# Performance work log

Hardware: AMD Instinct MI355X
Metric: run time of the kernel (lower is better)

Reference implementation:

```python
import jax, jax.numpy as jnp
import numpy as np

N, E, S, G = 524288, 2097152, 8192, 64
F_IN, HID = 64, 128


def setup_inputs() -> dict:
    key = jax.random.key(0)
    ks = jax.random.split(key, 12)
    x = jax.random.normal(ks[0], (N, F_IN), dtype=jnp.float32)
    edge_index = jax.random.randint(ks[1], (2, E), 0, N, dtype=jnp.int64)
    node_batch = jnp.sort(jax.random.randint(ks[2], (N,), 0, S, dtype=jnp.int64))
    weights = jax.random.uniform(ks[3], (S, 1), dtype=jnp.float32)
    subgraph_batch = jnp.sort(jax.random.randint(ks[4], (S,), 0, G, dtype=jnp.int64))
    s = 1.0 / np.sqrt(F_IN)
    h = 1.0 / np.sqrt(HID)
    W_l = jax.random.uniform(ks[5], (F_IN, HID), jnp.float32, -s, s)
    W_r = jax.random.uniform(ks[6], (F_IN, HID), jnp.float32, -s, s)
    b_conv = jax.random.uniform(ks[7], (HID,), jnp.float32, -s, s)
    W1 = jax.random.uniform(ks[8], (HID, HID), jnp.float32, -h, h)
    b1 = jax.random.uniform(ks[9], (HID,), jnp.float32, -h, h)
    W2 = jax.random.uniform(ks[10], (HID, 1), jnp.float32, -h, h)
    b2 = jax.random.uniform(ks[11], (1,), jnp.float32, -h, h)
    return {"x": x, "edge_index": edge_index, "node_batch": node_batch,
            "weights": weights, "subgraph_batch": subgraph_batch,
            "W_l": W_l, "W_r": W_r, "b_conv": b_conv,
            "W1": W1, "b1": b1, "W2": W2, "b2": b2}


def reference(x, edge_index, node_batch, weights, subgraph_batch,
              W_l, W_r, b_conv, W1, b1, W2, b2):
    src, dst = edge_index[0], edge_index[1]
    # GraphSAGE mean aggregation: gather neighbor feats, scatter-mean to dst
    msg_sum = jax.ops.segment_sum(x[src], dst, num_segments=N)  # [N, F_IN]
    deg = jax.ops.segment_sum(jnp.ones((E,), x.dtype), dst, num_segments=N)
    agg = msg_sum / jnp.maximum(deg, 1.0)[:, None]
    h = jax.nn.relu(agg @ W_l + x @ W_r + b_conv)               # [N, HID]
    # global_add_pool nodes -> subgraph embeddings
    g = jax.ops.segment_sum(h, node_batch, num_segments=S)      # [S, HID]
    # MLP head -> scalar per subgraph
    s = jax.nn.leaky_relu(g @ W1 + b1, negative_slope=0.01) @ W2 + b2  # [S, 1]
    sw = s * weights
    energy = jax.ops.segment_sum(sw, subgraph_batch, num_segments=G)   # [G, 1]
    norm = jax.ops.segment_sum(weights, subgraph_batch, num_segments=G)
    return energy / norm
```

## Files before the change

### kernel.cpp

```cpp
#include <hip/hip_runtime.h>
#include <hip/hip_bf16.h>

#define NN 524288
#define NE 2097152
#define NS 8192
#define NG 64
#define FIN 64
#define HIDDEN 128

#define NB 512
#define BIN_NODES 1024
#define CAP 4608

typedef __attribute__((ext_vector_type(8))) unsigned short ushort8;
typedef __attribute__((ext_vector_type(4))) unsigned short ushort4v;
typedef __attribute__((ext_vector_type(8))) short bf16x8;
typedef __attribute__((ext_vector_type(4))) float floatx4;

__device__ __forceinline__ unsigned short f2b(float f) {
  union { float f; unsigned int u; } c; c.f = f;
  unsigned int u = c.u;
  unsigned int r = (u + 0x7FFFu + ((u >> 16) & 1u)) >> 16;
  return (unsigned short)r;
}
__device__ __forceinline__ float b2f(unsigned short b) {
  union { unsigned int u; float f; } c; c.u = ((unsigned int)b) << 16;
  return c.f;
}

__global__ __launch_bounds__(256) void k_cast(const float* __restrict__ x,
                                              unsigned short* __restrict__ xb) {
  size_t i = ((size_t)blockIdx.x * 256 + threadIdx.x) * 8;
  float4 v0 = *(const float4*)(x + i);
  float4 v1 = *(const float4*)(x + i + 4);
  ushort8 r;
  r[0] = f2b(v0.x); r[1] = f2b(v0.y); r[2] = f2b(v0.z); r[3] = f2b(v0.w);
  r[4] = f2b(v1.x); r[5] = f2b(v1.y); r[6] = f2b(v1.z); r[7] = f2b(v1.w);
  *(ushort8*)(xb + i) = r;
}

__global__ __launch_bounds__(256) void k_prepw(const float* __restrict__ Wl,
                                               const float* __restrict__ Wr,
                                               unsigned short* __restrict__ Wt) {
  int i = blockIdx.x * 256 + threadIdx.x;
  int n = i >> 7, k = i & 127;
  float v = (k < FIN) ? Wl[k * HIDDEN + n] : Wr[(k - FIN) * HIDDEN + n];
  Wt[n * HIDDEN + k] = f2b(v);
}

__global__ __launch_bounds__(256) void k_bin1(const int* __restrict__ ei,
                                              int* __restrict__ binCursor,
                                              unsigned int* __restrict__ pairs) {
  __shared__ unsigned int pk[4096];
  __shared__ unsigned short bn[4096];
  __shared__ int cnt[NB];
  __shared__ int base[NB];
  const int t = threadIdx.x;
  const int eBase = blockIdx.x * 4096;
  cnt[t] = 0; cnt[t + 256] = 0;
  __syncthreads();
#pragma unroll
  for (int i = 0; i < 16; ++i) {
    int j = i * 256 + t;
    int e = eBase + j;
    int src = ei[e];
    int dst = ei[NE + e];
    int bin = dst >> 10;
    pk[j] = ((unsigned int)(dst & 1023) << 19) | (unsigned int)src;
    bn[j] = (unsigned short)bin;
    atomicAdd(&cnt[bin], 1);
  }
  __syncthreads();
  {
    int c0 = cnt[t], c1 = cnt[t + 256];
    base[t]       = atomicAdd(&binCursor[t], c0);
    base[t + 256] = atomicAdd(&binCursor[t + 256], c1);
    cnt[t] = 0; cnt[t + 256] = 0;
  }
  __syncthreads();
#pragma unroll
  for (int i = 0; i < 16; ++i) {
    int j = i * 256 + t;
    int bin = bn[j];
    int ofs = atomicAdd(&cnt[bin], 1);
    pairs[(size_t)bin * CAP + base[bin] + ofs] = pk[j];
  }
}

__global__ __launch_bounds__(256) void k_bin2(const int* __restrict__ binCursor,
                                              unsigned int* __restrict__ pairs,
                                              int* __restrict__ S) {
  __shared__ unsigned int pk[CAP];
  __shared__ int cnt[BIN_NODES];
  __shared__ int ps[256];
  const int t = threadIdx.x;
  const int b = blockIdx.x;
  int total = binCursor[b];
  if (total > CAP) total = CAP;
  const int gbase = b * CAP;

  for (int i = t; i < total; i += 256) pk[i] = pairs[gbase + i];
  cnt[t] = 0; cnt[t + 256] = 0; cnt[t + 512] = 0; cnt[t + 768] = 0;
  __syncthreads();

  for (int i = t; i < total; i += 256) atomicAdd(&cnt[pk[i] >> 19], 1);
  __syncthreads();

  int c0 = cnt[4 * t], c1 = cnt[4 * t + 1], c2 = cnt[4 * t + 2], c3 = cnt[4 * t + 3];
  int tot4 = c0 + c1 + c2 + c3;
  ps[t] = tot4;
  __syncthreads();
  for (int off = 1; off < 256; off <<= 1) {
    int v = 0;
    if (t >= off) v = ps[t - off];
    __syncthreads();
    ps[t] += v;
    __syncthreads();
  }
  int e0 = ps[t] - tot4;
  int e1 = e0 + c0, e2 = e1 + c1, e3 = e2 + c2;
  cnt[4 * t] = e0; cnt[4 * t + 1] = e1; cnt[4 * t + 2] = e2; cnt[4 * t + 3] = e3;
  int sidx = b * (BIN_NODES + 1) + 4 * t;
  S[sidx]     = gbase + e0;
  S[sidx + 1] = gbase + e1;
  S[sidx + 2] = gbase + e2;
  S[sidx + 3] = gbase + e3;
  if (t == 0) S[b * (BIN_NODES + 1) + BIN_NODES] = gbase + total;
  __syncthreads();

  for (int i = t; i < total; i += 256) {
    unsigned int p = pk[i];
    int dl = p >> 19;
    int ofs = atomicAdd(&cnt[dl], 1);
    pairs[gbase + ofs] = p & 0x7FFFFu;
  }
}

__global__ __launch_bounds__(256) void k_aggregate(const unsigned short* __restrict__ xb,
                                                   const int* __restrict__ S,
                                                   const unsigned int* __restrict__ bucket,
                                                   unsigned short* __restrict__ msgb) {
  const int t = threadIdx.x;
  const int grp = t >> 3;
  const int lane = t & 7;
  const int n = blockIdx.x * 32 + grp;
  const int sidx = n + (n >> 10);
  const int rp0 = S[sidx];
  const int rp1 = S[sidx + 1];

  float a0[8] = {0,0,0,0,0,0,0,0};
  float a1[8] = {0,0,0,0,0,0,0,0};
  float a2[8] = {0,0,0,0,0,0,0,0};
  float a3[8] = {0,0,0,0,0,0,0,0};
  int e = rp0;
  for (; e + 3 < rp1; e += 4) {
    int s0 = bucket[e], s1 = bucket[e + 1], s2 = bucket[e + 2], s3 = bucket[e + 3];
    ushort8 v0 = *(const ushort8*)(xb + (size_t)s0 * FIN + (lane << 3));
    ushort8 v1 = *(const ushort8*)(xb + (size_t)s1 * FIN + (lane << 3));
    ushort8 v2 = *(const ushort8*)(xb + (size_t)s2 * FIN + (lane << 3));
    ushort8 v3 = *(const ushort8*)(xb + (size_t)s3 * FIN + (lane << 3));
#pragma unroll
    for (int j = 0; j < 8; ++j) {
      a0[j] += b2f(v0[j]); a1[j] += b2f(v1[j]);
      a2[j] += b2f(v2[j]); a3[j] += b2f(v3[j]);
    }
  }
  for (; e < rp1; ++e) {
    int s0 = bucket[e];
    ushort8 v0 = *(const ushort8*)(xb + (size_t)s0 * FIN + (lane << 3));
#pragma unroll
    for (int j = 0; j < 8; ++j) a0[j] += b2f(v0[j]);
  }
  float rdeg = 1.f / fmaxf((float)(rp1 - rp0), 1.f);
  ushort8 r;
#pragma unroll
  for (int j = 0; j < 8; ++j)
    r[j] = f2b((a0[j] + a1[j] + a2[j] + a3[j]) * rdeg);
  *(ushort8*)(msgb + (size_t)n * FIN + (lane << 3)) = r;
}

#define CB_NODES 128
__global__ __launch_bounds__(512, 6) void k_conv(const unsigned short* __restrict__ msgb,
                                                 const unsigned short* __restrict__ xb,
                                                 const int* __restrict__ node_batch,
                                                 const unsigned short* __restrict__ Wt,
                                                 const float* __restrict__ bconv,
                                                 float* __restrict__ g) {
  __shared__ unsigned short As[128 * 136];
  __shared__ int nb_s[CB_NODES];
  const int t = threadIdx.x;
  const int n0 = blockIdx.x * CB_NODES;

  if (t < CB_NODES) nb_s[t] = node_batch[n0 + t];

#pragma unroll
  for (int it = 0; it < 4; ++it) {
    int i = it * 512 + t;
    int n = i >> 4;
    int c = i & 15;
    const unsigned short* src = (c < 8)
        ? msgb + (size_t)(n0 + n) * FIN + c * 8
        : xb + (size_t)(n0 + n) * FIN + (c - 8) * 8;
    *(ushort8*)(As + n * 136 + c * 8) = *(const ushort8*)src;
  }

  const int wave = t >> 6;
  const int lane = t & 63;
  const int l16 = lane & 15;
  const int quad = lane >> 4;

  bf16x8 bfrag[4];
#pragma unroll
  for (int ks = 0; ks < 4; ++ks)
    bfrag[ks] = *(const bf16x8*)(Wt + (size_t)(wave * 16 + l16) * HIDDEN + ks * 32 + quad * 8);
  float bv = bconv[wave * 16 + l16];

  floatx4 acc[8];
#pragma unroll
  for (int mt = 0; mt < 8; ++mt) acc[mt] = (floatx4){0.f, 0.f, 0.f, 0.f};

  __syncthreads();

#pragma unroll
  for (int mt = 0; mt < 8; ++mt) {
#pragma unroll
    for (int ks = 0; ks < 4; ++ks) {
      bf16x8 a = *(const bf16x8*)(As + (mt * 16 + l16) * 136 + ks * 32 + quad * 8);
      acc[mt] = __builtin_amdgcn_mfma_f32_16x16x32_bf16(a, bfrag[ks], acc[mt], 0, 0, 0);
    }
  }

  __syncthreads();

  {
    int col = wave * 16 + l16;
#pragma unroll
    for (int mt = 0; mt < 8; ++mt)
#pragma unroll
      for (int r = 0; r < 4; ++r) {
        int row = mt * 16 + quad * 4 + r;
        float hv = fmaxf(acc[mt][r] + bv, 0.f);
        As[row * 136 + col] = f2b(hv);
      }
  }
  __syncthreads();

  {
    int j = t & 127;
    int q = t >> 7;
    int ns = q * 32, ne = ns + 32;
    float sum = 0.f;
    int cur = nb_s[ns];
    for (int n = ns; n < ne; ++n) {
      int b = nb_s[n];
      if (b != cur) {
        unsafeAtomicAdd(&g[(size_t)cur * HIDDEN + j], sum);
        sum = 0.f;
        cur = b;
      }
      sum += b2f(As[n * 136 + j]);
    }
    unsafeAtomicAdd(&g[(size_t)cur * HIDDEN + j], sum);
  }
}

__global__ __launch_bounds__(256) void k_head(const float* __restrict__ g,
                                              const float* __restrict__ W1,
                                              const float* __restrict__ b1,
                                              const float* __restrict__ W2,
                                              const float* __restrict__ b2,
                                              const float* __restrict__ wts,
                                              const int* __restrict__ sgb,
                                              float* __restrict__ egy,
                                              float* __restrict__ nrm) {
  int s = blockIdx.x * 4 + (threadIdx.x >> 6);
  int lane = threadIdx.x & 63;
  const float* grow = g + (size_t)s * HIDDEN;
  float acc0 = b1[lane];
  float acc1 = b1[lane + 64];
  for (int k = 0; k < HIDDEN; ++k) {
    float gk = grow[k];
    acc0 = fmaf(gk, W1[k * HIDDEN + lane], acc0);
    acc1 = fmaf(gk, W1[k * HIDDEN + 64 + lane], acc1);
  }
  float t0 = acc0 > 0.f ? acc0 : 0.01f * acc0;
  float t1 = acc1 > 0.f ? acc1 : 0.01f * acc1;
  float part = t0 * W2[lane] + t1 * W2[lane + 64];
#pragma unroll
  for (int off = 32; off > 0; off >>= 1) part += __shfl_down(part, off, 64);
  if (lane == 0) {
    float sval = part + b2[0];
    float w = wts[s];
    int grp = sgb[s];
    unsafeAtomicAdd(&egy[grp], sval * w);
    unsafeAtomicAdd(&nrm[grp], w);
  }
}

__global__ void k_final(const float* __restrict__ egy,
                        const float* __restrict__ nrm,
                        float* __restrict__ out) {
  int t = threadIdx.x;
  out[t] = egy[t] / nrm[t];
}

extern "C" void kernel_launch(void* const* d_in, const int* in_sizes, int n_in,
                              void* d_out, int out_size, void* d_ws, size_t ws_size,
                              hipStream_t stream) {
  const float* x   = (const float*)d_in[0];
  const int*   ei  = (const int*)d_in[1];
  const int*   nb  = (const int*)d_in[2];
  const float* wts = (const float*)d_in[3];
  const int*   sgb = (const int*)d_in[4];
  const float* Wl  = (const float*)d_in[5];
  const float* Wr  = (const float*)d_in[6];
  const float* bcv = (const float*)d_in[7];
  const float* W1  = (const float*)d_in[8];
  const float* b1  = (const float*)d_in[9];
  const float* W2  = (const float*)d_in[10];
  const float* b2  = (const float*)d_in[11];
  float* out = (float*)d_out;

  int*   binCursor = (int*)d_ws;
  float* g         = (float*)(binCursor + NB);
  float* egy       = g + (size_t)NS * HIDDEN;
  float* nrm       = egy + NG;
  int*   S         = (int*)(nrm + NG);
  unsigned int* pairs = (unsigned int*)(S + NB * (BIN_NODES + 1));
  unsigned short* xb   = (unsigned short*)(pairs + (size_t)NB * CAP);
  unsigned short* msgb = xb + (size_t)NN * FIN;
  unsigned short* Wt   = msgb + (size_t)NN * FIN;

  size_t zero_bytes = ((size_t)NB + (size_t)NS * HIDDEN + 2 * NG) * 4;
  hipMemsetAsync(d_ws, 0, zero_bytes, stream);

  k_cast <<<(NN * FIN) / (256 * 8), 256, 0, stream>>>(x, xb);
  k_prepw<<<64, 256, 0, stream>>>(Wl, Wr, Wt);
  k_bin1 <<<NE / 4096, 256, 0, stream>>>(ei, binCursor, pairs);
  k_bin2 <<<NB, 256, 0, stream>>>(binCursor, pairs, S);
  k_aggregate<<<NN / 32, 256, 0, stream>>>(xb, S, pairs, msgb);
  k_conv<<<NN / CB_NODES, 512, 0, stream>>>(msgb, xb, nb, Wt, bcv, g);
  k_head<<<NS / 4, 256, 0, stream>>>(g, W1, b1, W2, b2, wts, sgb, egy, nrm);
  k_final<<<1, 64, 0, stream>>>(egy, nrm, out);
}
```

Before: 441.3 us.

## Fuse neighbor mean aggregation into conv kernel via shared-memory tile

The separate aggregation kernel is removed. Each conv block now gathers and averages neighbor features for its 128 nodes directly into the shared-memory A tile, beside the self features. This avoids writing and re-reading the bf16 message buffer through global memory and saves one kernel launch. In exchange the gather latency now sits inside the conv kernel, which runs at higher register pressure and lower occupancy, and the four separate accumulators are folded into one.

After: 420.4 us. 4.7% less time.

```diff
diff --git a/kernel.cpp b/kernel.cpp
--- a/kernel.cpp
+++ b/kernel.cpp
@@ -13,7 +13,6 @@
 #define CAP 4608
 
 typedef __attribute__((ext_vector_type(8))) unsigned short ushort8;
-typedef __attribute__((ext_vector_type(4))) unsigned short ushort4v;
 typedef __attribute__((ext_vector_type(8))) short bf16x8;
 typedef __attribute__((ext_vector_type(4))) float floatx4;
 
@@ -136,56 +135,14 @@
   }
 }
 
-__global__ __launch_bounds__(256) void k_aggregate(const unsigned short* __restrict__ xb,
-                                                   const int* __restrict__ S,
-                                                   const unsigned int* __restrict__ bucket,
-                                                   unsigned short* __restrict__ msgb) {
-  const int t = threadIdx.x;
-  const int grp = t >> 3;
-  const int lane = t & 7;
-  const int n = blockIdx.x * 32 + grp;
-  const int sidx = n + (n >> 10);
-  const int rp0 = S[sidx];
-  const int rp1 = S[sidx + 1];
-
-  float a0[8] = {0,0,0,0,0,0,0,0};
-  float a1[8] = {0,0,0,0,0,0,0,0};
-  float a2[8] = {0,0,0,0,0,0,0,0};
-  float a3[8] = {0,0,0,0,0,0,0,0};
-  int e = rp0;
-  for (; e + 3 < rp1; e += 4) {
-    int s0 = bucket[e], s1 = bucket[e + 1], s2 = bucket[e + 2], s3 = bucket[e + 3];
-    ushort8 v0 = *(const ushort8*)(xb + (size_t)s0 * FIN + (lane << 3));
-    ushort8 v1 = *(const ushort8*)(xb + (size_t)s1 * FIN + (lane << 3));
-    ushort8 v2 = *(const ushort8*)(xb + (size_t)s2 * FIN + (lane << 3));
-    ushort8 v3 = *(const ushort8*)(xb + (size_t)s3 * FIN + (lane << 3));
-#pragma unroll
-    for (int j = 0; j < 8; ++j) {
-      a0[j] += b2f(v0[j]); a1[j] += b2f(v1[j]);
-      a2[j] += b2f(v2[j]); a3[j] += b2f(v3[j]);
-    }
-  }
-  for (; e < rp1; ++e) {
-    int s0 = bucket[e];
-    ushort8 v0 = *(const ushort8*)(xb + (size_t)s0 * FIN + (lane << 3));
-#pragma unroll
-    for (int j = 0; j < 8; ++j) a0[j] += b2f(v0[j]);
-  }
-  float rdeg = 1.f / fmaxf((float)(rp1 - rp0), 1.f);
-  ushort8 r;
-#pragma unroll
-  for (int j = 0; j < 8; ++j)
-    r[j] = f2b((a0[j] + a1[j] + a2[j] + a3[j]) * rdeg);
-  *(ushort8*)(msgb + (size_t)n * FIN + (lane << 3)) = r;
-}
-
 #define CB_NODES 128
-__global__ __launch_bounds__(512, 6) void k_conv(const unsigned short* __restrict__ msgb,
-                                                 const unsigned short* __restrict__ xb,
-                                                 const int* __restrict__ node_batch,
-                                                 const unsigned short* __restrict__ Wt,
-                                                 const float* __restrict__ bconv,
-                                                 float* __restrict__ g) {
+__global__ __launch_bounds__(512, 6) void k_aggconv(const unsigned short* __restrict__ xb,
+                                                    const int* __restrict__ S,
+                                                    const unsigned int* __restrict__ bucket,
+                                                    const int* __restrict__ node_batch,
+                                                    const unsigned short* __restrict__ Wt,
+                                                    const float* __restrict__ bconv,
+                                                    float* __restrict__ g) {
   __shared__ unsigned short As[128 * 136];
   __shared__ int nb_s[CB_NODES];
   const int t = threadIdx.x;
@@ -194,14 +151,48 @@
   if (t < CB_NODES) nb_s[t] = node_batch[n0 + t];
 
 #pragma unroll
-  for (int it = 0; it < 4; ++it) {
+  for (int it = 0; it < 2; ++it) {
     int i = it * 512 + t;
-    int n = i >> 4;
-    int c = i & 15;
-    const unsigned short* src = (c < 8)
-        ? msgb + (size_t)(n0 + n) * FIN + c * 8
-        : xb + (size_t)(n0 + n) * FIN + (c - 8) * 8;
-    *(ushort8*)(As + n * 136 + c * 8) = *(const ushort8*)src;
+    int n = i >> 3;
+    int c = i & 7;
+    *(ushort8*)(As + n * 136 + 64 + c * 8) =
+        *(const ushort8*)(xb + (size_t)(n0 + n) * FIN + c * 8);
+  }
+
+  {
+    const int lane8 = t & 7;
+    const int grp = t >> 3;
+#pragma unroll
+    for (int p = 0; p < 2; ++p) {
+      int nl = p * 64 + grp;
+      int n = n0 + nl;
+      int sidx = n + (n >> 10);
+      int rp0 = S[sidx];
+      int rp1 = S[sidx + 1];
+      float a[8] = {0,0,0,0,0,0,0,0};
+      int e = rp0;
+      for (; e + 3 < rp1; e += 4) {
+        int s0 = bucket[e], s1 = bucket[e + 1], s2 = bucket[e + 2], s3 = bucket[e + 3];
+        ushort8 v0 = *(const ushort8*)(xb + (size_t)s0 * FIN + (lane8 << 3));
+        ushort8 v1 = *(const ushort8*)(xb + (size_t)s1 * FIN + (lane8 << 3));
+        ushort8 v2 = *(const ushort8*)(xb + (size_t)s2 * FIN + (lane8 << 3));
+        ushort8 v3 = *(const ushort8*)(xb + (size_t)s3 * FIN + (lane8 << 3));
+#pragma unroll
+        for (int j = 0; j < 8; ++j)
+          a[j] += (b2f(v0[j]) + b2f(v1[j])) + (b2f(v2[j]) + b2f(v3[j]));
+      }
+      for (; e < rp1; ++e) {
+        int s0 = bucket[e];
+        ushort8 v0 = *(const ushort8*)(xb + (size_t)s0 * FIN + (lane8 << 3));
+#pragma unroll
+        for (int j = 0; j < 8; ++j) a[j] += b2f(v0[j]);
+      }
+      float rdeg = 1.f / fmaxf((float)(rp1 - rp0), 1.f);
+      ushort8 r;
+#pragma unroll
+      for (int j = 0; j < 8; ++j) r[j] = f2b(a[j] * rdeg);
+      *(ushort8*)(As + nl * 136 + lane8 * 8) = r;
+    }
   }
 
   const int wave = t >> 6;
@@ -328,8 +319,7 @@
   int*   S         = (int*)(nrm + NG);
   unsigned int* pairs = (unsigned int*)(S + NB * (BIN_NODES + 1));
   unsigned short* xb   = (unsigned short*)(pairs + (size_t)NB * CAP);
-  unsigned short* msgb = xb + (size_t)NN * FIN;
-  unsigned short* Wt   = msgb + (size_t)NN * FIN;
+  unsigned short* Wt   = xb + (size_t)NN * FIN;
 
   size_t zero_bytes = ((size_t)NB + (size_t)NS * HIDDEN + 2 * NG) * 4;
   hipMemsetAsync(d_ws, 0, zero_bytes, stream);
@@ -338,8 +328,7 @@
   k_prepw<<<64, 256, 0, stream>>>(Wl, Wr, Wt);
   k_bin1 <<<NE / 4096, 256, 0, stream>>>(ei, binCursor, pairs);
   k_bin2 <<<NB, 256, 0, stream>>>(binCursor, pairs, S);
-  k_aggregate<<<NN / 32, 256, 0, stream>>>(xb, S, pairs, msgb);
-  k_conv<<<NN / CB_NODES, 512, 0, stream>>>(msgb, xb, nb, Wt, bcv, g);
+  k_aggconv<<<NN / CB_NODES, 512, 0, stream>>>(xb, S, pairs, nb, Wt, bcv, g);
   k_head<<<NS / 4, 256, 0, stream>>>(g, W1, b1, W2, b2, wts, sgb, egy, nrm);
   k_final<<<1, 64, 0, stream>>>(egy, nrm, out);
 }
```
